# Performance work log

Measured on AMD Instinct MI355X. Metric: run time of the kernel, lower is better.

The kernel has to match this reference:

```python
import jax, jax.numpy as jnp
import numpy as np

N = 100000
E = 1600000
IN_FEATS = 512
H1, F1 = 8, 8          # layer1: 8 heads x 8 units
H2, F2 = 1, 40         # layer2: 1 head x out_feats
NEG_SLOPE = 0.2


def setup_inputs() -> dict:
    key = jax.random.key(0)
    ks = jax.random.split(key, 12)
    x = jax.random.normal(ks[0], (N, IN_FEATS), dtype=jnp.float32)
    src = jax.random.randint(ks[1], (E,), 0, N, dtype=jnp.int32)
    dst = jax.random.randint(ks[2], (E,), 0, N, dtype=jnp.int32)
    # Xavier-ish init for params
    W1 = jax.random.normal(ks[3], (IN_FEATS, H1 * F1), dtype=jnp.float32) * (1.0 / np.sqrt(IN_FEATS))
    al1 = jax.random.normal(ks[4], (H1, F1), dtype=jnp.float32) * 0.1
    ar1 = jax.random.normal(ks[5], (H1, F1), dtype=jnp.float32) * 0.1
    b1 = jnp.zeros((H1 * F1,), dtype=jnp.float32)
    W2 = jax.random.normal(ks[6], (H1 * F1, H2 * F2), dtype=jnp.float32) * (1.0 / np.sqrt(H1 * F1))
    al2 = jax.random.normal(ks[7], (H2, F2), dtype=jnp.float32) * 0.1
    ar2 = jax.random.normal(ks[8], (H2, F2), dtype=jnp.float32) * 0.1
    b2 = jnp.zeros((H2 * F2,), dtype=jnp.float32)
    return {"x": x, "src": src, "dst": dst,
            "W1": W1, "al1": al1, "ar1": ar1, "b1": b1,
            "W2": W2, "al2": al2, "ar2": ar2, "b2": b2}


def _gat_conv(feat, src, dst, W, al, ar, b, activation):
    """DGL-style GATConv (dropout disabled / eval mode)."""
    n = feat.shape[0]
    heads, fdim = al.shape
    h = (feat @ W).reshape(n, heads, fdim)            # [N, H, F]
    el = jnp.einsum('nhf,hf->nh', h, al)              # [N, H]
    er = jnp.einsum('nhf,hf->nh', h, ar)              # [N, H]
    e = jax.nn.leaky_relu(el[src] + er[dst], NEG_SLOPE)   # [E, H]
    # edge softmax over incoming edges of each dst node (numerically stable)
    m = jax.ops.segment_max(e, dst, num_segments=n)   # [N, H]
    ex = jnp.exp(e - m[dst])
    s = jax.ops.segment_sum(ex, dst, num_segments=n)  # [N, H]
    alpha = ex / s[dst]                               # [E, H]
    msg = h[src] * alpha[:, :, None]                  # [E, H, F]
    rst = jax.ops.segment_sum(msg, dst, num_segments=n)  # [N, H, F]
    rst = rst + b.reshape(1, heads, fdim)
    if activation is not None:
        rst = activation(rst)
    return rst


def reference(x, src, dst, W1, al1, ar1, b1, W2, al2, ar2, b2):
    h1 = _gat_conv(x, src, dst, W1, al1, ar1, b1, jax.nn.elu)   # [N, H1, F1]
    h1 = h1.reshape(x.shape[0], H1 * F1)                        # flatten(1)
    h2 = _gat_conv(h1, src, dst, W2, al2, ar2, b2, None)        # [N, 1, F2]
    logits = h2.mean(axis=1)                                    # [N, F2]
    return jax.nn.log_softmax(logits, axis=1)
```

## Files before the change

### kernel.cpp

```cpp
#include <hip/hip_runtime.h>
#include <cstdint>
#include <cstddef>

#define IN_F 512
#define C1 64
#define NH 8
#define FD 8
#define C2 40
#define NEG 0.2f

typedef __attribute__((ext_vector_type(8))) short bf16x8;
typedef __attribute__((ext_vector_type(4))) float f32x4;

__device__ inline unsigned short f32_to_bf16_rne(float f) {
    unsigned int u = __float_as_uint(f);
    unsigned int r = (u + 0x7FFFu + ((u >> 16) & 1u)) >> 16;
    return (unsigned short)r;
}
__device__ inline float bf16_to_f32(unsigned short s) {
    return __uint_as_float(((unsigned int)s) << 16);
}

__global__ __launch_bounds__(256) void hist_k(const int* __restrict__ dst, int* __restrict__ deg,
                                              int* __restrict__ pos, int E) {
    int e = blockIdx.x * 256 + threadIdx.x;
    if (e < E) pos[e] = atomicAdd(&deg[dst[e]], 1);
}

__global__ __launch_bounds__(1024) void scan_local_k(const int* __restrict__ deg, int* __restrict__ rowp,
                                                     int* __restrict__ bsums, int n) {
    __shared__ int tmp[1024];
    int tx = threadIdx.x;
    int i = blockIdx.x * 1024 + tx;
    int v = (i < n) ? deg[i] : 0;
    tmp[tx] = v;
    __syncthreads();
    for (int d = 1; d < 1024; d <<= 1) {
        int t = (tx >= d) ? tmp[tx - d] : 0;
        __syncthreads();
        tmp[tx] += t;
        __syncthreads();
    }
    if (i < n) rowp[i] = tmp[tx] - v;
    if (tx == 1023) bsums[blockIdx.x] = tmp[tx];
}

__global__ __launch_bounds__(1024) void scan_add_k(int* rowp, const int* __restrict__ bsums, int n, int nb) {
    __shared__ int red[128];
    int tx = threadIdx.x;
    if (tx < 128) red[tx] = (tx < blockIdx.x && tx < nb) ? bsums[tx] : 0;
    __syncthreads();
    if (tx < 64) red[tx] += red[tx + 64];
    __syncthreads();
    if (tx < 32) red[tx] += red[tx + 32];
    __syncthreads();
    if (tx < 16) red[tx] += red[tx + 16];
    __syncthreads();
    if (tx < 8) red[tx] += red[tx + 8];
    __syncthreads();
    if (tx < 4) red[tx] += red[tx + 4];
    __syncthreads();
    if (tx < 2) red[tx] += red[tx + 2];
    __syncthreads();
    if (tx == 0) red[0] += red[1];
    __syncthreads();
    int off = red[0];
    int i = blockIdx.x * 1024 + tx;
    if (i < n) rowp[i] += off;
}

__global__ __launch_bounds__(256) void scatter_k(const int* __restrict__ src, const int* __restrict__ dst,
                                                 const int* __restrict__ rowp, const int* __restrict__ pos,
                                                 int* __restrict__ csr_src, int E) {
    int e = blockIdx.x * 256 + threadIdx.x;
    if (e >= E) return;
    csr_src[rowp[dst[e]] + pos[e]] = src[e];
}

__global__ __launch_bounds__(256) void pre_k(const float* __restrict__ W1, const float* __restrict__ W2,
                                             unsigned short* __restrict__ wt_hi, unsigned short* __restrict__ wt_lo,
                                             unsigned short* __restrict__ w2t_hi, unsigned short* __restrict__ w2t_lo) {
    int id = blockIdx.x * 256 + threadIdx.x;
    if (id < IN_F * C1) {
        int col = id & (C1 - 1);
        int k = id >> 6;
        float w = W1[id];
        unsigned short hb = f32_to_bf16_rne(w);
        unsigned short lb = f32_to_bf16_rne(w - bf16_to_f32(hb));
        wt_hi[(size_t)col * IN_F + k] = hb;
        wt_lo[(size_t)col * IN_F + k] = lb;
    } else {
        int id2 = id - IN_F * C1;
        if (id2 < 48 * 64) {
            int c = id2 >> 6, k = id2 & 63;
            float w = (c < C2) ? W2[(size_t)k * C2 + c] : 0.f;
            unsigned short hb = f32_to_bf16_rne(w);
            unsigned short lb = f32_to_bf16_rne(w - bf16_to_f32(hb));
            w2t_hi[c * 64 + k] = hb;
            w2t_lo[c * 64 + k] = lb;
        }
    }
}

__global__ __launch_bounds__(256) void gemm1_mfma_k(const float* __restrict__ x,
                                                    const unsigned short* __restrict__ wt_hi,
                                                    const unsigned short* __restrict__ wt_lo,
                                                    const float* __restrict__ al, const float* __restrict__ ar,
                                                    unsigned short* __restrict__ hb_out,
                                                    float* __restrict__ el, float* __restrict__ er, int N) {
    __shared__ alignas(16) unsigned short wlds[2][8192];
    const int tid = threadIdx.x;
    const int wave = tid >> 6, lane = tid & 63;
    const int m = lane & 15, q = lane >> 4;
    const int row = blockIdx.x * 64 + wave * 16 + m;
    const int row_c = row < N ? row : N - 1;
    const float* xp = x + (size_t)row_c * IN_F + q * 8;

    f32x4 acc[4];
#pragma unroll
    for (int ct = 0; ct < 4; ct++) acc[ct] = (f32x4){0.f, 0.f, 0.f, 0.f};
    float4 xr[2][4];

#define WLOAD(c, buf)                                                                              \
    {                                                                                              \
        _Pragma("unroll") for (int j_ = 0; j_ < 4; j_++) {                                         \
            int slot_ = j_ * 256 + wave * 64 + lane;                                               \
            const unsigned short* gbase_ = (slot_ < 512) ? wt_hi : wt_lo;                          \
            int s_ = slot_ & 511;                                                                  \
            int col_ = s_ & 63, kq_ = s_ >> 6;                                                     \
            const unsigned short* g_ = gbase_ + (size_t)col_ * IN_F + (c) * 64 + kq_ * 8;          \
            unsigned short* l_ = &wlds[buf][0] + (size_t)(j_ * 256 + wave * 64) * 8;               \
            __builtin_amdgcn_global_load_lds((const __attribute__((address_space(1))) unsigned int*)g_, \
                                             (__attribute__((address_space(3))) unsigned int*)l_,  \
                                             16, 0, 0);                                            \
        }                                                                                          \
    }
#define XLOAD(c, r)                                  \
    {                                                \
        const float* xsrc_ = xp + (c) * 64;          \
        (r)[0] = *(const float4*)(xsrc_);            \
        (r)[1] = *(const float4*)(xsrc_ + 4);        \
        (r)[2] = *(const float4*)(xsrc_ + 32);       \
        (r)[3] = *(const float4*)(xsrc_ + 36);       \
    }

    WLOAD(0, 0);
    XLOAD(0, xr[0]);

    for (int c = 0; c < 8; c++) {
        int p = c & 1;
        __syncthreads();
        if (c < 7) {
            WLOAD(c + 1, p ^ 1);
            XLOAD(c + 1, xr[p ^ 1]);
        }
#pragma unroll
        for (int ki = 0; ki < 2; ki++) {
            float f[8];
            f[0] = xr[p][ki * 2].x; f[1] = xr[p][ki * 2].y; f[2] = xr[p][ki * 2].z; f[3] = xr[p][ki * 2].w;
            f[4] = xr[p][ki * 2 + 1].x; f[5] = xr[p][ki * 2 + 1].y; f[6] = xr[p][ki * 2 + 1].z; f[7] = xr[p][ki * 2 + 1].w;
            unsigned int u[8], lu[8];
#pragma unroll
            for (int j = 0; j < 8; j++) u[j] = __float_as_uint(f[j]);
            union { uint4 u4; bf16x8 v; } H, L;
            H.u4.x = __builtin_amdgcn_perm(u[1], u[0], 0x07060302u);
            H.u4.y = __builtin_amdgcn_perm(u[3], u[2], 0x07060302u);
            H.u4.z = __builtin_amdgcn_perm(u[5], u[4], 0x07060302u);
            H.u4.w = __builtin_amdgcn_perm(u[7], u[6], 0x07060302u);
#pragma unroll
            for (int j = 0; j < 8; j++)
                lu[j] = __float_as_uint(f[j] - __uint_as_float(u[j] & 0xFFFF0000u));
            L.u4.x = __builtin_amdgcn_perm(lu[1], lu[0], 0x07060302u);
            L.u4.y = __builtin_amdgcn_perm(lu[3], lu[2], 0x07060302u);
            L.u4.z = __builtin_amdgcn_perm(lu[5], lu[4], 0x07060302u);
            L.u4.w = __builtin_amdgcn_perm(lu[7], lu[6], 0x07060302u);
            int kq = ki * 4 + q;
#pragma unroll
            for (int ct = 0; ct < 4; ct++) {
                int slot = kq * 64 + ct * 16 + m;
                bf16x8 bh = *(const bf16x8*)&wlds[p][slot * 8];
                bf16x8 bl = *(const bf16x8*)&wlds[p][4096 + slot * 8];
                acc[ct] = __builtin_amdgcn_mfma_f32_16x16x32_bf16(H.v, bh, acc[ct], 0, 0, 0);
                acc[ct] = __builtin_amdgcn_mfma_f32_16x16x32_bf16(L.v, bh, acc[ct], 0, 0, 0);
                acc[ct] = __builtin_amdgcn_mfma_f32_16x16x32_bf16(H.v, bl, acc[ct], 0, 0, 0);
            }
        }
    }
    int rbase = blockIdx.x * 64 + wave * 16 + q * 4;
#pragma unroll
    for (int r = 0; r < 4; r++) {
        int ro = rbase + r;
        if (ro < N) {
#pragma unroll
            for (int ct = 0; ct < 4; ct++)
                hb_out[(size_t)ro * C1 + ct * 16 + m] = f32_to_bf16_rne(acc[ct][r]);
        }
    }

    __syncthreads();
    float* hst = (float*)&wlds[0][0];
    {
        int rr = wave * 16 + q * 4;
#pragma unroll
        for (int r = 0; r < 4; r++)
#pragma unroll
            for (int ct = 0; ct < 4; ct++)
                hst[(rr + r) * 69 + ct * 16 + m] = acc[ct][r];
    }
    __syncthreads();
    for (int id = tid; id < 512; id += 256) {
        int r = id >> 3, hd = id & 7;
        int nn = blockIdx.x * 64 + r;
        if (nn < N) {
            float e_l = 0.f, e_r = 0.f;
#pragma unroll
            for (int f = 0; f < 8; f++) {
                float v = hst[r * 69 + hd * 8 + f];
                e_l += v * al[hd * 8 + f];
                e_r += v * ar[hd * 8 + f];
            }
            el[(size_t)nn * NH + hd] = e_l;
            er[(size_t)nn * NH + hd] = e_r;
        }
    }
#undef WLOAD
#undef XLOAD
}

__global__ __launch_bounds__(256) void l1_wave_k(const unsigned short* __restrict__ hb,
                                                 const float* __restrict__ el, const float* __restrict__ er,
                                                 const int* __restrict__ rowp, const int* __restrict__ deg,
                                                 const int* __restrict__ csr_src, const float* __restrict__ b1,
                                                 float* __restrict__ h1out, int N) {
    int n = (blockIdx.x * 256 + threadIdx.x) >> 6;
    if (n >= N) return;
    int lane = threadIdx.x & 63;
    int q = lane >> 4;
    int f = lane & 15;
    int hd = f >> 1;
    int start = rowp[n], cnt = deg[n];
    float erd = er[(size_t)n * NH + hd];
    const uint2* hb64 = (const uint2*)hb;
    const int* cp = csr_src + start;
    float a0 = 0.f, a1 = 0.f, a2 = 0.f, a3 = 0.f, s = 0.f;
    if (cnt > 0) {
        int lastc = cnt - 1;
        int c0 = cp[(q < cnt) ? q : lastc];
        int c1 = cp[(4 + q < cnt) ? 4 + q : lastc];
        int i = 0;
        while (i + 8 < cnt) {
            int i8 = i + 8;
            int c2 = cp[(i8 + q < cnt) ? i8 + q : lastc];
            int c3 = cp[(i8 + 4 + q < cnt) ? i8 + 4 + q : lastc];
            float e0 = el[(size_t)c0 * NH + hd] + erd;
            float e1 = el[(size_t)c1 * NH + hd] + erd;
            uint2 v0 = hb64[(size_t)c0 * 16 + f];
            uint2 v1 = hb64[(size_t)c1 * 16 + f];
            e0 = e0 > 0.f ? e0 : NEG * e0;
            e1 = e1 > 0.f ? e1 : NEG * e1;
            float w0 = __expf(e0), w1 = __expf(e1);
            s += w0 + w1;
            a0 += w0 * __uint_as_float(v0.x << 16) + w1 * __uint_as_float(v1.x << 16);
            a1 += w0 * __uint_as_float(v0.x & 0xFFFF0000u) + w1 * __uint_as_float(v1.x & 0xFFFF0000u);
            a2 += w0 * __uint_as_float(v0.y << 16) + w1 * __uint_as_float(v1.y << 16);
            a3 += w0 * __uint_as_float(v0.y & 0xFFFF0000u) + w1 * __uint_as_float(v1.y & 0xFFFF0000u);
            c0 = c2; c1 = c3; i = i8;
        }
        {
            bool m0 = (i + q) < cnt, m1 = (i + 4 + q) < cnt;
            float e0 = el[(size_t)c0 * NH + hd] + erd;
            float e1 = el[(size_t)c1 * NH + hd] + erd;
            uint2 v0 = hb64[(size_t)c0 * 16 + f];
            uint2 v1 = hb64[(size_t)c1 * 16 + f];
            e0 = e0 > 0.f ? e0 : NEG * e0;
            e1 = e1 > 0.f ? e1 : NEG * e1;
            float w0 = m0 ? __expf(e0) : 0.f;
            float w1 = m1 ? __expf(e1) : 0.f;
            s += w0 + w1;
            a0 += w0 * __uint_as_float(v0.x << 16) + w1 * __uint_as_float(v1.x << 16);
            a1 += w0 * __uint_as_float(v0.x & 0xFFFF0000u) + w1 * __uint_as_float(v1.x & 0xFFFF0000u);
            a2 += w0 * __uint_as_float(v0.y << 16) + w1 * __uint_as_float(v1.y << 16);
            a3 += w0 * __uint_as_float(v0.y & 0xFFFF0000u) + w1 * __uint_as_float(v1.y & 0xFFFF0000u);
        }
    }
    a0 += __shfl_xor(a0, 16); a0 += __shfl_xor(a0, 32);
    a1 += __shfl_xor(a1, 16); a1 += __shfl_xor(a1, 32);
    a2 += __shfl_xor(a2, 16); a2 += __shfl_xor(a2, 32);
    a3 += __shfl_xor(a3, 16); a3 += __shfl_xor(a3, 32);
    s  += __shfl_xor(s, 16);  s  += __shfl_xor(s, 32);
    float sinv = (s > 0.f) ? 1.f / s : 0.f;
    float4 bv = *(const float4*)(b1 + f * 4);
    float o0 = a0 * sinv + bv.x;
    float o1 = a1 * sinv + bv.y;
    float o2 = a2 * sinv + bv.z;
    float o3 = a3 * sinv + bv.w;
    o0 = o0 > 0.f ? o0 : (__expf(o0) - 1.f);
    o1 = o1 > 0.f ? o1 : (__expf(o1) - 1.f);
    o2 = o2 > 0.f ? o2 : (__expf(o2) - 1.f);
    o3 = o3 > 0.f ? o3 : (__expf(o3) - 1.f);
    if (q == 0) *(float4*)(h1out + (size_t)n * C1 + f * 4) = make_float4(o0, o1, o2, o3);
}

__global__ __launch_bounds__(256) void gemm2_attn2_k(const float* __restrict__ h1,
                                                     const unsigned short* __restrict__ w2t_hi,
                                                     const unsigned short* __restrict__ w2t_lo,
                                                     const float* __restrict__ al2, const float* __restrict__ ar2,
                                                     unsigned short* __restrict__ h2b, float* __restrict__ el2,
                                                     float* __restrict__ er2, int N) {
    __shared__ float h2s[64][49];
    __shared__ float a2s[2 * C2];
    int t = threadIdx.x;
    int wave = t >> 6, lane = t & 63;
    int m = lane & 15, q = lane >> 4;
    int n0 = blockIdx.x * 64;
    if (t < C2) a2s[t] = al2[t];
    else if (t < 2 * C2) a2s[t] = ar2[t - C2];
    int row = n0 + wave * 16 + m;
    int row_c = row < N ? row : N - 1;
    const float* hp = h1 + (size_t)row_c * C1 + q * 8;
    f32x4 acc[3];
#pragma unroll
    for (int ct = 0; ct < 3; ct++) acc[ct] = (f32x4){0.f, 0.f, 0.f, 0.f};
#pragma unroll
    for (int ks = 0; ks < 2; ks++) {
        float4 r0 = *(const float4*)(hp + ks * 32);
        float4 r1 = *(const float4*)(hp + ks * 32 + 4);
        float f[8];
        f[0] = r0.x; f[1] = r0.y; f[2] = r0.z; f[3] = r0.w;
        f[4] = r1.x; f[5] = r1.y; f[6] = r1.z; f[7] = r1.w;
        unsigned int u[8], lu[8];
#pragma unroll
        for (int j = 0; j < 8; j++) u[j] = __float_as_uint(f[j]);
        union { uint4 u4; bf16x8 v; } H, L;
        H.u4.x = __builtin_amdgcn_perm(u[1], u[0], 0x07060302u);
        H.u4.y = __builtin_amdgcn_perm(u[3], u[2], 0x07060302u);
        H.u4.z = __builtin_amdgcn_perm(u[5], u[4], 0x07060302u);
        H.u4.w = __builtin_amdgcn_perm(u[7], u[6], 0x07060302u);
#pragma unroll
        for (int j = 0; j < 8; j++)
            lu[j] = __float_as_uint(f[j] - __uint_as_float(u[j] & 0xFFFF0000u));
        L.u4.x = __builtin_amdgcn_perm(lu[1], lu[0], 0x07060302u);
        L.u4.y = __builtin_amdgcn_perm(lu[3], lu[2], 0x07060302u);
        L.u4.z = __builtin_amdgcn_perm(lu[5], lu[4], 0x07060302u);
        L.u4.w = __builtin_amdgcn_perm(lu[7], lu[6], 0x07060302u);
        int kb = ks * 32 + q * 8;
#pragma unroll
        for (int ct = 0; ct < 3; ct++) {
            int col = ct * 16 + m;
            bf16x8 bh = *(const bf16x8*)(w2t_hi + col * 64 + kb);
            bf16x8 bl = *(const bf16x8*)(w2t_lo + col * 64 + kb);
            acc[ct] = __builtin_amdgcn_mfma_f32_16x16x32_bf16(H.v, bh, acc[ct], 0, 0, 0);
            acc[ct] = __builtin_amdgcn_mfma_f32_16x16x32_bf16(L.v, bh, acc[ct], 0, 0, 0);
            acc[ct] = __builtin_amdgcn_mfma_f32_16x16x32_bf16(H.v, bl, acc[ct], 0, 0, 0);
        }
    }
    int rl = wave * 16 + q * 4;
#pragma unroll
    for (int ct = 0; ct < 3; ct++)
#pragma unroll
        for (int r = 0; r < 4; r++) h2s[rl + r][ct * 16 + m] = acc[ct][r];
    __syncthreads();
    unsigned int* h2d = (unsigned int*)h2b;
    for (int o = t; o < 64 * 20; o += 256) {
        int r = o / 20, cd = o % 20;
        int nn = n0 + r;
        if (nn < N) {
            unsigned int lo16 = f32_to_bf16_rne(h2s[r][cd * 2]);
            unsigned int hi16 = f32_to_bf16_rne(h2s[r][cd * 2 + 1]);
            h2d[(size_t)nn * 20 + cd] = lo16 | (hi16 << 16);
        }
    }
    if (t < 64) {
        int nn = n0 + t;
        if (nn < N) {
            float e_l = 0.f, e_r = 0.f;
#pragma unroll
            for (int c = 0; c < C2; c++) {
                float v = h2s[t][c];
                e_l += v * a2s[c];
                e_r += v * a2s[C2 + c];
            }
            el2[nn] = e_l;
            er2[nn] = e_r;
        }
    }
}

__global__ __launch_bounds__(256) void l2_fused_k(const unsigned short* __restrict__ h2b,
                                                  const float* __restrict__ el, const float* __restrict__ er,
                                                  const int* __restrict__ rowp, const int* __restrict__ deg,
                                                  const int* __restrict__ csr_src, const float* __restrict__ b2,
                                                  float* __restrict__ out, int N) {
    int tid = threadIdx.x;
    int n = blockIdx.x * 32 + (tid >> 3);
    int sub = tid & 7;
    if (n >= N) return;
    float vals[8];
    if (sub < 5) {
        int start = rowp[n], cnt = deg[n];
        float erd = er[n];
        float s = 0.f;
        float acc[8];
#pragma unroll
        for (int j = 0; j < 8; j++) acc[j] = 0.f;
        const int* cp = csr_src + start;
        if (cnt > 0) {
            int last = cnt - 1;
            int c0 = cp[0];
            int c1 = cp[1 < cnt ? 1 : last];
            int c2 = cp[2 < cnt ? 2 : last];
            int c3 = cp[3 < cnt ? 3 : last];
            int i = 0;
            while (i + 4 < cnt) {
                int i4 = i + 4;
                int p0 = cp[i4];
                int p1 = cp[(i4 + 1 < cnt) ? i4 + 1 : last];
                int p2 = cp[(i4 + 2 < cnt) ? i4 + 2 : last];
                int p3 = cp[(i4 + 3 < cnt) ? i4 + 3 : last];
                float e0 = el[c0], e1 = el[c1], e2 = el[c2], e3 = el[c3];
                bf16x8 v0 = *(const bf16x8*)(h2b + (size_t)c0 * C2 + sub * 8);
                bf16x8 v1 = *(const bf16x8*)(h2b + (size_t)c1 * C2 + sub * 8);
                bf16x8 v2 = *(const bf16x8*)(h2b + (size_t)c2 * C2 + sub * 8);
                bf16x8 v3 = *(const bf16x8*)(h2b + (size_t)c3 * C2 + sub * 8);
                e0 += erd; e1 += erd; e2 += erd; e3 += erd;
                e0 = e0 > 0.f ? e0 : NEG * e0;
                e1 = e1 > 0.f ? e1 : NEG * e1;
                e2 = e2 > 0.f ? e2 : NEG * e2;
                e3 = e3 > 0.f ? e3 : NEG * e3;
                float w0 = __expf(e0), w1 = __expf(e1), w2 = __expf(e2), w3 = __expf(e3);
                s += (w0 + w1) + (w2 + w3);
#pragma unroll
                for (int j = 0; j < 8; j++) {
                    acc[j] += w0 * bf16_to_f32((unsigned short)v0[j]) + w1 * bf16_to_f32((unsigned short)v1[j]) +
                              w2 * bf16_to_f32((unsigned short)v2[j]) + w3 * bf16_to_f32((unsigned short)v3[j]);
                }
                c0 = p0; c1 = p1; c2 = p2; c3 = p3; i = i4;
            }
            {
                bool m0 = i < cnt, m1 = i + 1 < cnt, m2 = i + 2 < cnt, m3 = i + 3 < cnt;
                float e0 = el[c0], e1 = el[c1], e2 = el[c2], e3 = el[c3];
                bf16x8 v0 = *(const bf16x8*)(h2b + (size_t)c0 * C2 + sub * 8);
                bf16x8 v1 = *(const bf16x8*)(h2b + (size_t)c1 * C2 + sub * 8);
                bf16x8 v2 = *(const bf16x8*)(h2b + (size_t)c2 * C2 + sub * 8);
                bf16x8 v3 = *(const bf16x8*)(h2b + (size_t)c3 * C2 + sub * 8);
                e0 += erd; e1 += erd; e2 += erd; e3 += erd;
                e0 = e0 > 0.f ? e0 : NEG * e0;
                e1 = e1 > 0.f ? e1 : NEG * e1;
                e2 = e2 > 0.f ? e2 : NEG * e2;
                e3 = e3 > 0.f ? e3 : NEG * e3;
                float w0 = m0 ? __expf(e0) : 0.f;
                float w1 = m1 ? __expf(e1) : 0.f;
                float w2 = m2 ? __expf(e2) : 0.f;
                float w3 = m3 ? __expf(e3) : 0.f;
                s += (w0 + w1) + (w2 + w3);
#pragma unroll
                for (int j = 0; j < 8; j++) {
                    acc[j] += w0 * bf16_to_f32((unsigned short)v0[j]) + w1 * bf16_to_f32((unsigned short)v1[j]) +
                              w2 * bf16_to_f32((unsigned short)v2[j]) + w3 * bf16_to_f32((unsigned short)v3[j]);
                }
            }
        }
        float sinv = (s > 0.f) ? 1.f / s : 0.f;
        const float* bp = b2 + sub * 8;
#pragma unroll
        for (int j = 0; j < 8; j++) vals[j] = acc[j] * sinv + bp[j];
    } else {
#pragma unroll
        for (int j = 0; j < 8; j++) vals[j] = -1e30f;
    }
    float mx = vals[0];
#pragma unroll
    for (int j = 1; j < 8; j++) mx = fmaxf(mx, vals[j]);
#pragma unroll
    for (int off = 1; off < 8; off <<= 1) mx = fmaxf(mx, __shfl_xor(mx, off, 8));
    float se = 0.f;
#pragma unroll
    for (int j = 0; j < 8; j++) se += __expf(vals[j] - mx);
#pragma unroll
    for (int off = 1; off < 8; off <<= 1) se += __shfl_xor(se, off, 8);
    float ls = __logf(se) + mx;
    if (sub < 5) {
        float* op = out + (size_t)n * C2 + sub * 8;
        *(float4*)(op) = make_float4(vals[0] - ls, vals[1] - ls, vals[2] - ls, vals[3] - ls);
        *(float4*)(op + 4) = make_float4(vals[4] - ls, vals[5] - ls, vals[6] - ls, vals[7] - ls);
    }
}

extern "C" void kernel_launch(void* const* d_in, const int* in_sizes, int n_in,
                              void* d_out, int out_size, void* d_ws, size_t ws_size,
                              hipStream_t stream) {
    (void)n_in; (void)out_size; (void)ws_size;
    const float* x   = (const float*)d_in[0];
    const int*   src = (const int*)d_in[1];
    const int*   dst = (const int*)d_in[2];
    const float* W1  = (const float*)d_in[3];
    const float* al1 = (const float*)d_in[4];
    const float* ar1 = (const float*)d_in[5];
    const float* b1  = (const float*)d_in[6];
    const float* W2  = (const float*)d_in[7];
    const float* al2 = (const float*)d_in[8];
    const float* ar2 = (const float*)d_in[9];
    const float* b2  = (const float*)d_in[10];
    float* out = (float*)d_out;
    const int N = in_sizes[0] / IN_F;
    const int E = in_sizes[1];

    char* w = (char*)d_ws;
    auto alloc = [&](size_t bytes) -> char* {
        char* p = w;
        w += (bytes + 255) & ~(size_t)255;
        return p;
    };
    int* deg     = (int*)alloc((size_t)N * 4);
    int* rowp    = (int*)alloc((size_t)N * 4);
    int* bsums   = (int*)alloc(512);
    int* pos     = (int*)alloc((size_t)E * 4);
    int* csr_src = (int*)alloc((size_t)E * 4);
    unsigned short* wt_hi = (unsigned short*)alloc((size_t)IN_F * C1 * 2);
    unsigned short* wt_lo = (unsigned short*)alloc((size_t)IN_F * C1 * 2);
    unsigned short* w2t_hi = (unsigned short*)alloc((size_t)48 * 64 * 2);
    unsigned short* w2t_lo = (unsigned short*)alloc((size_t)48 * 64 * 2);
    unsigned short* hb    = (unsigned short*)alloc((size_t)N * C1 * 2);
    float* el1   = (float*)alloc((size_t)N * NH * 4);
    float* er1   = (float*)alloc((size_t)N * NH * 4);
    float* h1    = (float*)alloc((size_t)N * C1 * 4);
    unsigned short* h2b = (unsigned short*)alloc((size_t)N * C2 * 2);
    float* el2   = (float*)alloc((size_t)N * 4);
    float* er2   = (float*)alloc((size_t)N * 4);

    hipMemsetAsync(deg, 0, (size_t)N * 4, stream);

    int ebl = (E + 255) / 256;
    int nb = (N + 1023) / 1024;
    hist_k<<<ebl, 256, 0, stream>>>(dst, deg, pos, E);
    scan_local_k<<<nb, 1024, 0, stream>>>(deg, rowp, bsums, N);
    scan_add_k<<<nb, 1024, 0, stream>>>(rowp, bsums, N, nb);
    scatter_k<<<ebl, 256, 0, stream>>>(src, dst, rowp, pos, csr_src, E);

    pre_k<<<(IN_F * C1 + 48 * 64 + 255) / 256, 256, 0, stream>>>(W1, W2, wt_hi, wt_lo, w2t_hi, w2t_lo);
    gemm1_mfma_k<<<(N + 63) / 64, 256, 0, stream>>>(x, wt_hi, wt_lo, al1, ar1, hb, el1, er1, N);
    l1_wave_k<<<(N * 64 + 255) / 256, 256, 0, stream>>>(hb, el1, er1, rowp, deg, csr_src, b1, h1, N);
    gemm2_attn2_k<<<(N + 63) / 64, 256, 0, stream>>>(h1, w2t_hi, w2t_lo, al2, ar2, h2b, el2, er2, N);
    l2_fused_k<<<(N + 31) / 32, 256, 0, stream>>>(h2b, el2, er2, rowp, deg, csr_src, b2, out, N);
}
```

Baseline: 551.7 us.

## Fuse layer-1 aggregation with layer-2 GEMM and drop per-edge pos array

Merges the layer-1 edge aggregation kernel with the layer-2 projection GEMM. Each 1024-thread block aggregates 64 nodes into shared memory and then runs the MFMA GEMM from there, so the fp32 h1 tensor is no longer written to and re-read from global memory. The CSR build also drops the per-edge pos array: the scatter now takes slots with atomics on a copy of the row pointers. In exchange, the order of neighbours within each row becomes nondeterministic, so float summation order can vary between runs, and only 4 of the 16 waves do the GEMM phase.

```diff
diff --git a/kernel.cpp b/kernel.cpp
--- a/kernel.cpp
+++ b/kernel.cpp
@@ -21,10 +21,9 @@
     return __uint_as_float(((unsigned int)s) << 16);
 }
 
-__global__ __launch_bounds__(256) void hist_k(const int* __restrict__ dst, int* __restrict__ deg,
-                                              int* __restrict__ pos, int E) {
+__global__ __launch_bounds__(256) void hist_k(const int* __restrict__ dst, int* __restrict__ deg, int E) {
     int e = blockIdx.x * 256 + threadIdx.x;
-    if (e < E) pos[e] = atomicAdd(&deg[dst[e]], 1);
+    if (e < E) atomicAdd(&deg[dst[e]], 1);
 }
 
 __global__ __launch_bounds__(1024) void scan_local_k(const int* __restrict__ deg, int* __restrict__ rowp,
@@ -45,7 +44,8 @@
     if (tx == 1023) bsums[blockIdx.x] = tmp[tx];
 }
 
-__global__ __launch_bounds__(1024) void scan_add_k(int* rowp, const int* __restrict__ bsums, int n, int nb) {
+__global__ __launch_bounds__(1024) void scan_add_k(int* rowp, int* __restrict__ cur,
+                                                   const int* __restrict__ bsums, int n, int nb) {
     __shared__ int red[128];
     int tx = threadIdx.x;
     if (tx < 128) red[tx] = (tx < blockIdx.x && tx < nb) ? bsums[tx] : 0;
@@ -66,15 +66,19 @@
     __syncthreads();
     int off = red[0];
     int i = blockIdx.x * 1024 + tx;
-    if (i < n) rowp[i] += off;
+    if (i < n) {
+        int r = rowp[i] + off;
+        rowp[i] = r;
+        cur[i] = r;
+    }
 }
 
 __global__ __launch_bounds__(256) void scatter_k(const int* __restrict__ src, const int* __restrict__ dst,
-                                                 const int* __restrict__ rowp, const int* __restrict__ pos,
-                                                 int* __restrict__ csr_src, int E) {
+                                                 int* __restrict__ cur, int* __restrict__ csr_src, int E) {
     int e = blockIdx.x * 256 + threadIdx.x;
     if (e >= E) return;
-    csr_src[rowp[dst[e]] + pos[e]] = src[e];
+    int slot = atomicAdd(&cur[dst[e]], 1);
+    csr_src[slot] = src[e];
 }
 
 __global__ __launch_bounds__(256) void pre_k(const float* __restrict__ W1, const float* __restrict__ W2,
@@ -227,141 +231,147 @@
 #undef XLOAD
 }
 
-__global__ __launch_bounds__(256) void l1_wave_k(const unsigned short* __restrict__ hb,
-                                                 const float* __restrict__ el, const float* __restrict__ er,
-                                                 const int* __restrict__ rowp, const int* __restrict__ deg,
-                                                 const int* __restrict__ csr_src, const float* __restrict__ b1,
-                                                 float* __restrict__ h1out, int N) {
-    int n = (blockIdx.x * 256 + threadIdx.x) >> 6;
-    if (n >= N) return;
-    int lane = threadIdx.x & 63;
-    int q = lane >> 4;
-    int f = lane & 15;
-    int hd = f >> 1;
-    int start = rowp[n], cnt = deg[n];
-    float erd = er[(size_t)n * NH + hd];
-    const uint2* hb64 = (const uint2*)hb;
-    const int* cp = csr_src + start;
-    float a0 = 0.f, a1 = 0.f, a2 = 0.f, a3 = 0.f, s = 0.f;
-    if (cnt > 0) {
-        int lastc = cnt - 1;
-        int c0 = cp[(q < cnt) ? q : lastc];
-        int c1 = cp[(4 + q < cnt) ? 4 + q : lastc];
-        int i = 0;
-        while (i + 8 < cnt) {
-            int i8 = i + 8;
-            int c2 = cp[(i8 + q < cnt) ? i8 + q : lastc];
-            int c3 = cp[(i8 + 4 + q < cnt) ? i8 + 4 + q : lastc];
-            float e0 = el[(size_t)c0 * NH + hd] + erd;
-            float e1 = el[(size_t)c1 * NH + hd] + erd;
-            uint2 v0 = hb64[(size_t)c0 * 16 + f];
-            uint2 v1 = hb64[(size_t)c1 * 16 + f];
-            e0 = e0 > 0.f ? e0 : NEG * e0;
-            e1 = e1 > 0.f ? e1 : NEG * e1;
-            float w0 = __expf(e0), w1 = __expf(e1);
-            s += w0 + w1;
-            a0 += w0 * __uint_as_float(v0.x << 16) + w1 * __uint_as_float(v1.x << 16);
-            a1 += w0 * __uint_as_float(v0.x & 0xFFFF0000u) + w1 * __uint_as_float(v1.x & 0xFFFF0000u);
-            a2 += w0 * __uint_as_float(v0.y << 16) + w1 * __uint_as_float(v1.y << 16);
-            a3 += w0 * __uint_as_float(v0.y & 0xFFFF0000u) + w1 * __uint_as_float(v1.y & 0xFFFF0000u);
-            c0 = c2; c1 = c3; i = i8;
-        }
-        {
-            bool m0 = (i + q) < cnt, m1 = (i + 4 + q) < cnt;
-            float e0 = el[(size_t)c0 * NH + hd] + erd;
-            float e1 = el[(size_t)c1 * NH + hd] + erd;
-            uint2 v0 = hb64[(size_t)c0 * 16 + f];
-            uint2 v1 = hb64[(size_t)c1 * 16 + f];
-            e0 = e0 > 0.f ? e0 : NEG * e0;
-            e1 = e1 > 0.f ? e1 : NEG * e1;
-            float w0 = m0 ? __expf(e0) : 0.f;
-            float w1 = m1 ? __expf(e1) : 0.f;
-            s += w0 + w1;
-            a0 += w0 * __uint_as_float(v0.x << 16) + w1 * __uint_as_float(v1.x << 16);
-            a1 += w0 * __uint_as_float(v0.x & 0xFFFF0000u) + w1 * __uint_as_float(v1.x & 0xFFFF0000u);
-            a2 += w0 * __uint_as_float(v0.y << 16) + w1 * __uint_as_float(v1.y << 16);
-            a3 += w0 * __uint_as_float(v0.y & 0xFFFF0000u) + w1 * __uint_as_float(v1.y & 0xFFFF0000u);
-        }
-    }
-    a0 += __shfl_xor(a0, 16); a0 += __shfl_xor(a0, 32);
-    a1 += __shfl_xor(a1, 16); a1 += __shfl_xor(a1, 32);
-    a2 += __shfl_xor(a2, 16); a2 += __shfl_xor(a2, 32);
-    a3 += __shfl_xor(a3, 16); a3 += __shfl_xor(a3, 32);
-    s  += __shfl_xor(s, 16);  s  += __shfl_xor(s, 32);
-    float sinv = (s > 0.f) ? 1.f / s : 0.f;
-    float4 bv = *(const float4*)(b1 + f * 4);
-    float o0 = a0 * sinv + bv.x;
-    float o1 = a1 * sinv + bv.y;
-    float o2 = a2 * sinv + bv.z;
-    float o3 = a3 * sinv + bv.w;
-    o0 = o0 > 0.f ? o0 : (__expf(o0) - 1.f);
-    o1 = o1 > 0.f ? o1 : (__expf(o1) - 1.f);
-    o2 = o2 > 0.f ? o2 : (__expf(o2) - 1.f);
-    o3 = o3 > 0.f ? o3 : (__expf(o3) - 1.f);
-    if (q == 0) *(float4*)(h1out + (size_t)n * C1 + f * 4) = make_float4(o0, o1, o2, o3);
-}
-
-__global__ __launch_bounds__(256) void gemm2_attn2_k(const float* __restrict__ h1,
-                                                     const unsigned short* __restrict__ w2t_hi,
-                                                     const unsigned short* __restrict__ w2t_lo,
-                                                     const float* __restrict__ al2, const float* __restrict__ ar2,
-                                                     unsigned short* __restrict__ h2b, float* __restrict__ el2,
-                                                     float* __restrict__ er2, int N) {
+__global__ __launch_bounds__(1024) void l1_gemm2_k(const unsigned short* __restrict__ hb,
+                                                   const float* __restrict__ el, const float* __restrict__ er,
+                                                   const int* __restrict__ rowp, const int* __restrict__ deg,
+                                                   const int* __restrict__ csr_src, const float* __restrict__ b1,
+                                                   const unsigned short* __restrict__ w2t_hi,
+                                                   const unsigned short* __restrict__ w2t_lo,
+                                                   const float* __restrict__ al2, const float* __restrict__ ar2,
+                                                   unsigned short* __restrict__ h2b, float* __restrict__ el2,
+                                                   float* __restrict__ er2, int N) {
+    __shared__ float h1s[64][68];
     __shared__ float h2s[64][49];
     __shared__ float a2s[2 * C2];
     int t = threadIdx.x;
     int wave = t >> 6, lane = t & 63;
-    int m = lane & 15, q = lane >> 4;
     int n0 = blockIdx.x * 64;
     if (t < C2) a2s[t] = al2[t];
     else if (t < 2 * C2) a2s[t] = ar2[t - C2];
-    int row = n0 + wave * 16 + m;
-    int row_c = row < N ? row : N - 1;
-    const float* hp = h1 + (size_t)row_c * C1 + q * 8;
-    f32x4 acc[3];
-#pragma unroll
-    for (int ct = 0; ct < 3; ct++) acc[ct] = (f32x4){0.f, 0.f, 0.f, 0.f};
-#pragma unroll
-    for (int ks = 0; ks < 2; ks++) {
-        float4 r0 = *(const float4*)(hp + ks * 32);
-        float4 r1 = *(const float4*)(hp + ks * 32 + 4);
-        float f[8];
-        f[0] = r0.x; f[1] = r0.y; f[2] = r0.z; f[3] = r0.w;
-        f[4] = r1.x; f[5] = r1.y; f[6] = r1.z; f[7] = r1.w;
-        unsigned int u[8], lu[8];
-#pragma unroll
-        for (int j = 0; j < 8; j++) u[j] = __float_as_uint(f[j]);
-        union { uint4 u4; bf16x8 v; } H, L;
-        H.u4.x = __builtin_amdgcn_perm(u[1], u[0], 0x07060302u);
-        H.u4.y = __builtin_amdgcn_perm(u[3], u[2], 0x07060302u);
-        H.u4.z = __builtin_amdgcn_perm(u[5], u[4], 0x07060302u);
-        H.u4.w = __builtin_amdgcn_perm(u[7], u[6], 0x07060302u);
-#pragma unroll
-        for (int j = 0; j < 8; j++)
-            lu[j] = __float_as_uint(f[j] - __uint_as_float(u[j] & 0xFFFF0000u));
-        L.u4.x = __builtin_amdgcn_perm(lu[1], lu[0], 0x07060302u);
-        L.u4.y = __builtin_amdgcn_perm(lu[3], lu[2], 0x07060302u);
-        L.u4.z = __builtin_amdgcn_perm(lu[5], lu[4], 0x07060302u);
-        L.u4.w = __builtin_amdgcn_perm(lu[7], lu[6], 0x07060302u);
-        int kb = ks * 32 + q * 8;
-#pragma unroll
-        for (int ct = 0; ct < 3; ct++) {
-            int col = ct * 16 + m;
-            bf16x8 bh = *(const bf16x8*)(w2t_hi + col * 64 + kb);
-            bf16x8 bl = *(const bf16x8*)(w2t_lo + col * 64 + kb);
-            acc[ct] = __builtin_amdgcn_mfma_f32_16x16x32_bf16(H.v, bh, acc[ct], 0, 0, 0);
-            acc[ct] = __builtin_amdgcn_mfma_f32_16x16x32_bf16(L.v, bh, acc[ct], 0, 0, 0);
-            acc[ct] = __builtin_amdgcn_mfma_f32_16x16x32_bf16(H.v, bl, acc[ct], 0, 0, 0);
-        }
-    }
-    int rl = wave * 16 + q * 4;
-#pragma unroll
-    for (int ct = 0; ct < 3; ct++)
-#pragma unroll
-        for (int r = 0; r < 4; r++) h2s[rl + r][ct * 16 + m] = acc[ct][r];
-    __syncthreads();
+
+    int q = lane >> 4;
+    int f = lane & 15;
+    int hd = f >> 1;
+    const uint2* hb64 = (const uint2*)hb;
+
+    for (int k = 0; k < 4; k++) {
+        int r = wave * 4 + k;
+        int n = n0 + r;
+        float o0 = 0.f, o1 = 0.f, o2 = 0.f, o3 = 0.f;
+        if (n < N) {
+            int start = rowp[n], cnt = deg[n];
+            float erd = er[(size_t)n * NH + hd];
+            const int* cp = csr_src + start;
+            float a0 = 0.f, a1 = 0.f, a2 = 0.f, a3 = 0.f, s = 0.f;
+            if (cnt > 0) {
+                int lastc = cnt - 1;
+                int c0 = cp[(q < cnt) ? q : lastc];
+                int c1 = cp[(4 + q < cnt) ? 4 + q : lastc];
+                int i = 0;
+                while (i + 8 < cnt) {
+                    int i8 = i + 8;
+                    int c2 = cp[(i8 + q < cnt) ? i8 + q : lastc];
+                    int c3 = cp[(i8 + 4 + q < cnt) ? i8 + 4 + q : lastc];
+                    float e0 = el[(size_t)c0 * NH + hd] + erd;
+                    float e1 = el[(size_t)c1 * NH + hd] + erd;
+                    uint2 v0 = hb64[(size_t)c0 * 16 + f];
+                    uint2 v1 = hb64[(size_t)c1 * 16 + f];
+                    e0 = e0 > 0.f ? e0 : NEG * e0;
+                    e1 = e1 > 0.f ? e1 : NEG * e1;
+                    float w0 = __expf(e0), w1 = __expf(e1);
+                    s += w0 + w1;
+                    a0 += w0 * __uint_as_float(v0.x << 16) + w1 * __uint_as_float(v1.x << 16);
+                    a1 += w0 * __uint_as_float(v0.x & 0xFFFF0000u) + w1 * __uint_as_float(v1.x & 0xFFFF0000u);
+                    a2 += w0 * __uint_as_float(v0.y << 16) + w1 * __uint_as_float(v1.y << 16);
+                    a3 += w0 * __uint_as_float(v0.y & 0xFFFF0000u) + w1 * __uint_as_float(v1.y & 0xFFFF0000u);
+                    c0 = c2; c1 = c3; i = i8;
+                }
+                {
+                    bool m0 = (i + q) < cnt, m1 = (i + 4 + q) < cnt;
+                    float e0 = el[(size_t)c0 * NH + hd] + erd;
+                    float e1 = el[(size_t)c1 * NH + hd] + erd;
+                    uint2 v0 = hb64[(size_t)c0 * 16 + f];
+                    uint2 v1 = hb64[(size_t)c1 * 16 + f];
+                    e0 = e0 > 0.f ? e0 : NEG * e0;
+                    e1 = e1 > 0.f ? e1 : NEG * e1;
+                    float w0 = m0 ? __expf(e0) : 0.f;
+                    float w1 = m1 ? __expf(e1) : 0.f;
+                    s += w0 + w1;
+                    a0 += w0 * __uint_as_float(v0.x << 16) + w1 * __uint_as_float(v1.x << 16);
+                    a1 += w0 * __uint_as_float(v0.x & 0xFFFF0000u) + w1 * __uint_as_float(v1.x & 0xFFFF0000u);
+                    a2 += w0 * __uint_as_float(v0.y << 16) + w1 * __uint_as_float(v1.y << 16);
+                    a3 += w0 * __uint_as_float(v0.y & 0xFFFF0000u) + w1 * __uint_as_float(v1.y & 0xFFFF0000u);
+                }
+            }
+            a0 += __shfl_xor(a0, 16); a0 += __shfl_xor(a0, 32);
+            a1 += __shfl_xor(a1, 16); a1 += __shfl_xor(a1, 32);
+            a2 += __shfl_xor(a2, 16); a2 += __shfl_xor(a2, 32);
+            a3 += __shfl_xor(a3, 16); a3 += __shfl_xor(a3, 32);
+            s  += __shfl_xor(s, 16);  s  += __shfl_xor(s, 32);
+            float sinv = (s > 0.f) ? 1.f / s : 0.f;
+            float4 bv = *(const float4*)(b1 + f * 4);
+            o0 = a0 * sinv + bv.x;
+            o1 = a1 * sinv + bv.y;
+            o2 = a2 * sinv + bv.z;
+            o3 = a3 * sinv + bv.w;
+            o0 = o0 > 0.f ? o0 : (__expf(o0) - 1.f);
+            o1 = o1 > 0.f ? o1 : (__expf(o1) - 1.f);
+            o2 = o2 > 0.f ? o2 : (__expf(o2) - 1.f);
+            o3 = o3 > 0.f ? o3 : (__expf(o3) - 1.f);
+        }
+        if (q == 0) *(float4*)&h1s[r][f * 4] = make_float4(o0, o1, o2, o3);
+    }
+    __syncthreads();
+
+    if (wave < 4) {
+        int m = lane & 15, qq = lane >> 4;
+        f32x4 acc[3];
+#pragma unroll
+        for (int ct = 0; ct < 3; ct++) acc[ct] = (f32x4){0.f, 0.f, 0.f, 0.f};
+#pragma unroll
+        for (int ks = 0; ks < 2; ks++) {
+            const float* hp = &h1s[wave * 16 + m][qq * 8 + ks * 32];
+            float4 r0 = *(const float4*)hp;
+            float4 r1 = *(const float4*)(hp + 4);
+            float ff[8];
+            ff[0] = r0.x; ff[1] = r0.y; ff[2] = r0.z; ff[3] = r0.w;
+            ff[4] = r1.x; ff[5] = r1.y; ff[6] = r1.z; ff[7] = r1.w;
+            unsigned int u[8], lu[8];
+#pragma unroll
+            for (int j = 0; j < 8; j++) u[j] = __float_as_uint(ff[j]);
+            union { uint4 u4; bf16x8 v; } H, L;
+            H.u4.x = __builtin_amdgcn_perm(u[1], u[0], 0x07060302u);
+            H.u4.y = __builtin_amdgcn_perm(u[3], u[2], 0x07060302u);
+            H.u4.z = __builtin_amdgcn_perm(u[5], u[4], 0x07060302u);
+            H.u4.w = __builtin_amdgcn_perm(u[7], u[6], 0x07060302u);
+#pragma unroll
+            for (int j = 0; j < 8; j++)
+                lu[j] = __float_as_uint(ff[j] - __uint_as_float(u[j] & 0xFFFF0000u));
+            L.u4.x = __builtin_amdgcn_perm(lu[1], lu[0], 0x07060302u);
+            L.u4.y = __builtin_amdgcn_perm(lu[3], lu[2], 0x07060302u);
+            L.u4.z = __builtin_amdgcn_perm(lu[5], lu[4], 0x07060302u);
+            L.u4.w = __builtin_amdgcn_perm(lu[7], lu[6], 0x07060302u);
+            int kb = ks * 32 + qq * 8;
+#pragma unroll
+            for (int ct = 0; ct < 3; ct++) {
+                int col = ct * 16 + m;
+                bf16x8 bh = *(const bf16x8*)(w2t_hi + col * 64 + kb);
+                bf16x8 bl = *(const bf16x8*)(w2t_lo + col * 64 + kb);
+                acc[ct] = __builtin_amdgcn_mfma_f32_16x16x32_bf16(H.v, bh, acc[ct], 0, 0, 0);
+                acc[ct] = __builtin_amdgcn_mfma_f32_16x16x32_bf16(L.v, bh, acc[ct], 0, 0, 0);
+                acc[ct] = __builtin_amdgcn_mfma_f32_16x16x32_bf16(H.v, bl, acc[ct], 0, 0, 0);
+            }
+        }
+        int rl = wave * 16 + qq * 4;
+#pragma unroll
+        for (int ct = 0; ct < 3; ct++)
+#pragma unroll
+            for (int r = 0; r < 4; r++) h2s[rl + r][ct * 16 + m] = acc[ct][r];
+    }
+    __syncthreads();
+
     unsigned int* h2d = (unsigned int*)h2b;
-    for (int o = t; o < 64 * 20; o += 256) {
+    for (int o = t; o < 64 * 20; o += 1024) {
         int r = o / 20, cd = o % 20;
         int nn = n0 + r;
         if (nn < N) {
@@ -513,8 +523,8 @@
     };
     int* deg     = (int*)alloc((size_t)N * 4);
     int* rowp    = (int*)alloc((size_t)N * 4);
+    int* cur     = (int*)alloc((size_t)N * 4);
     int* bsums   = (int*)alloc(512);
-    int* pos     = (int*)alloc((size_t)E * 4);
     int* csr_src = (int*)alloc((size_t)E * 4);
     unsigned short* wt_hi = (unsigned short*)alloc((size_t)IN_F * C1 * 2);
     unsigned short* wt_lo = (unsigned short*)alloc((size_t)IN_F * C1 * 2);
@@ -523,7 +533,6 @@
     unsigned short* hb    = (unsigned short*)alloc((size_t)N * C1 * 2);
     float* el1   = (float*)alloc((size_t)N * NH * 4);
     float* er1   = (float*)alloc((size_t)N * NH * 4);
-    float* h1    = (float*)alloc((size_t)N * C1 * 4);
     unsigned short* h2b = (unsigned short*)alloc((size_t)N * C2 * 2);
     float* el2   = (float*)alloc((size_t)N * 4);
     float* er2   = (float*)alloc((size_t)N * 4);
@@ -532,14 +541,14 @@
 
     int ebl = (E + 255) / 256;
     int nb = (N + 1023) / 1024;
-    hist_k<<<ebl, 256, 0, stream>>>(dst, deg, pos, E);
+    hist_k<<<ebl, 256, 0, stream>>>(dst, deg, E);
     scan_local_k<<<nb, 1024, 0, stream>>>(deg, rowp, bsums, N);
-    scan_add_k<<<nb, 1024, 0, stream>>>(rowp, bsums, N, nb);
-    scatter_k<<<ebl, 256, 0, stream>>>(src, dst, rowp, pos, csr_src, E);
+    scan_add_k<<<nb, 1024, 0, stream>>>(rowp, cur, bsums, N, nb);
+    scatter_k<<<ebl, 256, 0, stream>>>(src, dst, cur, csr_src, E);
 
     pre_k<<<(IN_F * C1 + 48 * 64 + 255) / 256, 256, 0, stream>>>(W1, W2, wt_hi, wt_lo, w2t_hi, w2t_lo);
     gemm1_mfma_k<<<(N + 63) / 64, 256, 0, stream>>>(x, wt_hi, wt_lo, al1, ar1, hb, el1, er1, N);
-    l1_wave_k<<<(N * 64 + 255) / 256, 256, 0, stream>>>(hb, el1, er1, rowp, deg, csr_src, b1, h1, N);
-    gemm2_attn2_k<<<(N + 63) / 64, 256, 0, stream>>>(h1, w2t_hi, w2t_lo, al2, ar2, h2b, el2, er2, N);
+    l1_gemm2_k<<<(N + 63) / 64, 1024, 0, stream>>>(hb, el1, er1, rowp, deg, csr_src, b1,
+                                                   w2t_hi, w2t_lo, al2, ar2, h2b, el2, er2, N);
     l2_fused_k<<<(N + 31) / 32, 256, 0, stream>>>(h2b, el2, er2, rowp, deg, csr_src, b2, out, N);
 }
```

Result: slower. 627.0 us (+13.7%).

## Merge independent CSR-build and weight-prep kernels via block-range dispatch

Applied to the files above, without the earlier changes.

The histogram kernel and the weight-split preprocessing kernel become one launch, with blocks partitioned by index. The CSR scatter is likewise merged into the first GEMM kernel, so the scatter blocks and the GEMM blocks run concurrently. Each edge block now handles four edges per thread. This cuts launch count and lets independent work overlap, at the cost of scatter blocks reserving the GEMM's LDS allocation, which may limit occupancy.

```diff
diff --git a/kernel.cpp b/kernel.cpp
--- a/kernel.cpp
+++ b/kernel.cpp
@@ -21,66 +21,21 @@
     return __uint_as_float(((unsigned int)s) << 16);
 }
 
-__global__ __launch_bounds__(256) void hist_k(const int* __restrict__ dst, int* __restrict__ deg,
-                                              int* __restrict__ pos, int E) {
-    int e = blockIdx.x * 256 + threadIdx.x;
-    if (e < E) pos[e] = atomicAdd(&deg[dst[e]], 1);
-}
-
-__global__ __launch_bounds__(1024) void scan_local_k(const int* __restrict__ deg, int* __restrict__ rowp,
-                                                     int* __restrict__ bsums, int n) {
-    __shared__ int tmp[1024];
-    int tx = threadIdx.x;
-    int i = blockIdx.x * 1024 + tx;
-    int v = (i < n) ? deg[i] : 0;
-    tmp[tx] = v;
-    __syncthreads();
-    for (int d = 1; d < 1024; d <<= 1) {
-        int t = (tx >= d) ? tmp[tx - d] : 0;
-        __syncthreads();
-        tmp[tx] += t;
-        __syncthreads();
-    }
-    if (i < n) rowp[i] = tmp[tx] - v;
-    if (tx == 1023) bsums[blockIdx.x] = tmp[tx];
-}
-
-__global__ __launch_bounds__(1024) void scan_add_k(int* rowp, const int* __restrict__ bsums, int n, int nb) {
-    __shared__ int red[128];
-    int tx = threadIdx.x;
-    if (tx < 128) red[tx] = (tx < blockIdx.x && tx < nb) ? bsums[tx] : 0;
-    __syncthreads();
-    if (tx < 64) red[tx] += red[tx + 64];
-    __syncthreads();
-    if (tx < 32) red[tx] += red[tx + 32];
-    __syncthreads();
-    if (tx < 16) red[tx] += red[tx + 16];
-    __syncthreads();
-    if (tx < 8) red[tx] += red[tx + 8];
-    __syncthreads();
-    if (tx < 4) red[tx] += red[tx + 4];
-    __syncthreads();
-    if (tx < 2) red[tx] += red[tx + 2];
-    __syncthreads();
-    if (tx == 0) red[0] += red[1];
-    __syncthreads();
-    int off = red[0];
-    int i = blockIdx.x * 1024 + tx;
-    if (i < n) rowp[i] += off;
-}
-
-__global__ __launch_bounds__(256) void scatter_k(const int* __restrict__ src, const int* __restrict__ dst,
-                                                 const int* __restrict__ rowp, const int* __restrict__ pos,
-                                                 int* __restrict__ csr_src, int E) {
-    int e = blockIdx.x * 256 + threadIdx.x;
-    if (e >= E) return;
-    csr_src[rowp[dst[e]] + pos[e]] = src[e];
-}
-
-__global__ __launch_bounds__(256) void pre_k(const float* __restrict__ W1, const float* __restrict__ W2,
-                                             unsigned short* __restrict__ wt_hi, unsigned short* __restrict__ wt_lo,
-                                             unsigned short* __restrict__ w2t_hi, unsigned short* __restrict__ w2t_lo) {
-    int id = blockIdx.x * 256 + threadIdx.x;
+__global__ __launch_bounds__(256) void hist_pre_k(const int* __restrict__ dst, int* __restrict__ deg,
+                                                  int* __restrict__ pos, int E, int HB,
+                                                  const float* __restrict__ W1, const float* __restrict__ W2,
+                                                  unsigned short* __restrict__ wt_hi, unsigned short* __restrict__ wt_lo,
+                                                  unsigned short* __restrict__ w2t_hi, unsigned short* __restrict__ w2t_lo) {
+    if ((int)blockIdx.x < HB) {
+        int base = blockIdx.x * 1024 + threadIdx.x;
+#pragma unroll
+        for (int j = 0; j < 4; j++) {
+            int e = base + j * 256;
+            if (e < E) pos[e] = atomicAdd(&deg[dst[e]], 1);
+        }
+        return;
+    }
+    int id = (blockIdx.x - HB) * 256 + threadIdx.x;
     if (id < IN_F * C1) {
         int col = id & (C1 - 1);
         int k = id >> 6;
@@ -102,17 +57,72 @@
     }
 }
 
-__global__ __launch_bounds__(256) void gemm1_mfma_k(const float* __restrict__ x,
+__global__ __launch_bounds__(1024) void scan_local_k(const int* __restrict__ deg, int* __restrict__ rowp,
+                                                     int* __restrict__ bsums, int n) {
+    __shared__ int tmp[1024];
+    int tx = threadIdx.x;
+    int i = blockIdx.x * 1024 + tx;
+    int v = (i < n) ? deg[i] : 0;
+    tmp[tx] = v;
+    __syncthreads();
+    for (int d = 1; d < 1024; d <<= 1) {
+        int t = (tx >= d) ? tmp[tx - d] : 0;
+        __syncthreads();
+        tmp[tx] += t;
+        __syncthreads();
+    }
+    if (i < n) rowp[i] = tmp[tx] - v;
+    if (tx == 1023) bsums[blockIdx.x] = tmp[tx];
+}
+
+__global__ __launch_bounds__(1024) void scan_add_k(int* rowp, const int* __restrict__ bsums, int n, int nb) {
+    __shared__ int red[128];
+    int tx = threadIdx.x;
+    if (tx < 128) red[tx] = (tx < blockIdx.x && tx < nb) ? bsums[tx] : 0;
+    __syncthreads();
+    if (tx < 64) red[tx] += red[tx + 64];
+    __syncthreads();
+    if (tx < 32) red[tx] += red[tx + 32];
+    __syncthreads();
+    if (tx < 16) red[tx] += red[tx + 16];
+    __syncthreads();
+    if (tx < 8) red[tx] += red[tx + 8];
+    __syncthreads();
+    if (tx < 4) red[tx] += red[tx + 4];
+    __syncthreads();
+    if (tx < 2) red[tx] += red[tx + 2];
+    __syncthreads();
+    if (tx == 0) red[0] += red[1];
+    __syncthreads();
+    int off = red[0];
+    int i = blockIdx.x * 1024 + tx;
+    if (i < n) rowp[i] += off;
+}
+
+__global__ __launch_bounds__(256) void scat_gemm1_k(const int* __restrict__ src, const int* __restrict__ dst,
+                                                    const int* __restrict__ rowp, const int* __restrict__ pos,
+                                                    int* __restrict__ csr_src, int E, int SB,
+                                                    const float* __restrict__ x,
                                                     const unsigned short* __restrict__ wt_hi,
                                                     const unsigned short* __restrict__ wt_lo,
                                                     const float* __restrict__ al, const float* __restrict__ ar,
                                                     unsigned short* __restrict__ hb_out,
                                                     float* __restrict__ el, float* __restrict__ er, int N) {
     __shared__ alignas(16) unsigned short wlds[2][8192];
+    if ((int)blockIdx.x < SB) {
+        int base = blockIdx.x * 1024 + threadIdx.x;
+#pragma unroll
+        for (int j = 0; j < 4; j++) {
+            int e = base + j * 256;
+            if (e < E) csr_src[rowp[dst[e]] + pos[e]] = src[e];
+        }
+        return;
+    }
+    const int gb = blockIdx.x - SB;
     const int tid = threadIdx.x;
     const int wave = tid >> 6, lane = tid & 63;
     const int m = lane & 15, q = lane >> 4;
-    const int row = blockIdx.x * 64 + wave * 16 + m;
+    const int row = gb * 64 + wave * 16 + m;
     const int row_c = row < N ? row : N - 1;
     const float* xp = x + (size_t)row_c * IN_F + q * 8;
 
@@ -186,7 +196,7 @@
             }
         }
     }
-    int rbase = blockIdx.x * 64 + wave * 16 + q * 4;
+    int rbase = gb * 64 + wave * 16 + q * 4;
 #pragma unroll
     for (int r = 0; r < 4; r++) {
         int ro = rbase + r;
@@ -210,7 +220,7 @@
     __syncthreads();
     for (int id = tid; id < 512; id += 256) {
         int r = id >> 3, hd = id & 7;
-        int nn = blockIdx.x * 64 + r;
+        int nn = gb * 64 + r;
         if (nn < N) {
             float e_l = 0.f, e_r = 0.f;
 #pragma unroll
@@ -530,16 +540,17 @@
 
     hipMemsetAsync(deg, 0, (size_t)N * 4, stream);
 
-    int ebl = (E + 255) / 256;
+    int HB = (E + 1023) / 1024;
+    int PREB = (IN_F * C1 + 48 * 64 + 255) / 256;
+    int GB = (N + 63) / 64;
     int nb = (N + 1023) / 1024;
-    hist_k<<<ebl, 256, 0, stream>>>(dst, deg, pos, E);
+
+    hist_pre_k<<<HB + PREB, 256, 0, stream>>>(dst, deg, pos, E, HB, W1, W2, wt_hi, wt_lo, w2t_hi, w2t_lo);
     scan_local_k<<<nb, 1024, 0, stream>>>(deg, rowp, bsums, N);
     scan_add_k<<<nb, 1024, 0, stream>>>(rowp, bsums, N, nb);
-    scatter_k<<<ebl, 256, 0, stream>>>(src, dst, rowp, pos, csr_src, E);
-
-    pre_k<<<(IN_F * C1 + 48 * 64 + 255) / 256, 256, 0, stream>>>(W1, W2, wt_hi, wt_lo, w2t_hi, w2t_lo);
-    gemm1_mfma_k<<<(N + 63) / 64, 256, 0, stream>>>(x, wt_hi, wt_lo, al1, ar1, hb, el1, er1, N);
+    scat_gemm1_k<<<HB + GB, 256, 0, stream>>>(src, dst, rowp, pos, csr_src, E, HB,
+                                              x, wt_hi, wt_lo, al1, ar1, hb, el1, er1, N);
     l1_wave_k<<<(N * 64 + 255) / 256, 256, 0, stream>>>(hb, el1, er1, rowp, deg, csr_src, b1, h1, N);
-    gemm2_attn2_k<<<(N + 63) / 64, 256, 0, stream>>>(h1, w2t_hi, w2t_lo, al2, ar2, h2b, el2, er2, N);
+    gemm2_attn2_k<<<GB, 256, 0, stream>>>(h1, w2t_hi, w2t_lo, al2, ar2, h2b, el2, er2, N);
     l2_fused_k<<<(N + 31) / 32, 256, 0, stream>>>(h2b, el2, er2, rowp, deg, csr_src, b2, out, N);
 }
```

New measurement: 544.8 us. No clear change (-1.2%).
